# Optimization experiments

Measured on AMD Instinct MI355X. Metric: run time of the kernel, lower is better.

Reference implementation:

```python
import jax, jax.numpy as jnp
import numpy as np

N_NODES = 100000
N_EDGES = 1600000
IN_DIM = 3
LATENT = 128
LATENT_DEC = 128
NUM_LAYER = 2      # shared-weight middle GCN layers
NUM_LAYER_DEC = 2  # shared-weight middle decoder layers


def _glorot(key, shape):
    fan_in, fan_out = shape[0], shape[1]
    lim = np.sqrt(6.0 / (fan_in + fan_out)).astype(np.float32)
    return jax.random.uniform(key, shape, jnp.float32, -lim, lim)


def setup_inputs() -> dict:
    key = jax.random.key(0)
    ks = jax.random.split(key, 10)
    x = jax.random.normal(ks[0], (N_NODES, IN_DIM), jnp.float32)
    edge_index = jax.random.randint(ks[1], (2, N_EDGES), 0, N_NODES, jnp.int64)
    return {
        "x": x,
        "edge_index": edge_index,
        "W_s": _glorot(ks[2], (IN_DIM, LATENT)),   "b_s": jnp.zeros((LATENT,), jnp.float32),
        "W_m": _glorot(ks[3], (LATENT, LATENT)),   "b_m": jnp.zeros((LATENT,), jnp.float32),
        "W_e": _glorot(ks[4], (LATENT, LATENT)),   "b_e": jnp.zeros((LATENT,), jnp.float32),
        "W_sd": _glorot(ks[5], (LATENT, LATENT_DEC)),    "b_sd": jnp.zeros((LATENT_DEC,), jnp.float32),
        "W_md": _glorot(ks[6], (LATENT_DEC, LATENT_DEC)),"b_md": jnp.zeros((LATENT_DEC,), jnp.float32),
        "W_ed": _glorot(ks[7], (LATENT_DEC, IN_DIM)),    "b_ed": jnp.zeros((IN_DIM,), jnp.float32),
    }


def _gcn_conv(h, W, b, src, dst, dinv):
    # PyG GCNConv: out_i = sum_j norm_ij * (x_j @ W) + b, norm = d^-1/2_i d^-1/2_j
    h = h @ W
    norm = dinv[src] * dinv[dst]                       # [E+N]
    msg = norm[:, None] * h[src]                       # gather + scale
    out = jax.ops.segment_sum(msg, dst, num_segments=N_NODES)  # scatter-add
    return out + b


def reference(x, edge_index, W_s, b_s, W_m, b_m, W_e, b_e, W_sd, b_sd, W_md, b_md, W_ed, b_ed):
    loops = jnp.arange(N_NODES, dtype=edge_index.dtype)
    src = jnp.concatenate([edge_index[0], loops])      # add self-loops
    dst = jnp.concatenate([edge_index[1], loops])
    deg = jax.ops.segment_sum(jnp.ones(src.shape[0], x.dtype), dst, num_segments=N_NODES)
    dinv = jnp.where(deg > 0, jax.lax.rsqrt(deg), 0.0)

    h = jax.nn.relu(_gcn_conv(x, W_s, b_s, src, dst, dinv))
    for _ in range(NUM_LAYER):  # shared weights (ModuleList([layer]*n))
        h = jax.nn.relu(_gcn_conv(h, W_m, b_m, src, dst, dinv))
    h = jax.nn.relu(_gcn_conv(h, W_e, b_e, src, dst, dinv))

    h = jax.nn.relu(h @ W_sd + b_sd)
    for _ in range(NUM_LAYER_DEC):  # shared weights
        h = jax.nn.relu(h @ W_md + b_md)
    y = h @ W_ed + b_ed
    return y + x
```

## Files before the change

### kernel.cpp

```cpp
#include <hip/hip_runtime.h>


typedef __attribute__((ext_vector_type(8))) short short8;
typedef __attribute__((ext_vector_type(4))) float floatx4;
typedef __attribute__((ext_vector_type(2))) float floatx2;

#define BIN_CH 8192
#define NBMAX 512

__device__ __forceinline__ unsigned short f2bf(float f) {
    unsigned int u = __float_as_uint(f);
    u += 0x7fffu + ((u >> 16) & 1u);
    return (unsigned short)(u >> 16);
}
__device__ __forceinline__ float bflo(unsigned int u) { return __uint_as_float(u << 16); }
__device__ __forceinline__ float bfhi(unsigned int u) { return __uint_as_float(u & 0xffff0000u); }
__device__ __forceinline__ unsigned char f2fp8(float f) {
    return (unsigned char)(__builtin_amdgcn_cvt_pk_fp8_f32(f, f, 0, false) & 0xFF);
}


__global__ __launch_bounds__(512) void bin_kernel(
        const int* __restrict__ src, const int* __restrict__ dst,
        int* __restrict__ gfill, unsigned int* __restrict__ binbuf,
        int NB, int C, int E) {
    __shared__ int hist[NBMAX];
    __shared__ int start[NBMAX];
    __shared__ int dstoff[NBMAX];
    int tid = threadIdx.x;
    int e0 = blockIdx.x * BIN_CH;
    for (int i = tid; i < NB; i += 512) hist[i] = 0;
    __syncthreads();
    for (int i = tid; i < BIN_CH; i += 512) {
        int e = e0 + i;
        if (e < E) atomicAdd(&hist[dst[e] >> 9], 1);
    }
    __syncthreads();
    if (tid < 64) {
        int carry = 0;
        for (int base = 0; base < NB; base += 64) {
            int idx = base + tid;
            int v = (idx < NB) ? hist[idx] : 0;
            int s = v;
            #pragma unroll
            for (int off = 1; off < 64; off <<= 1) {
                int u = __shfl_up(s, off);
                if (tid >= off) s += u;
            }
            if (idx < NB) start[idx] = carry + s - v;
            carry += __shfl(s, 63);
        }
    }
    __syncthreads();
    for (int i = tid; i < NB; i += 512) {
        int cnt = hist[i];
        int g = cnt ? atomicAdd(&gfill[i], cnt) : 0;
        dstoff[i] = g - start[i];
        hist[i] = start[i];
    }
    __syncthreads();
    for (int i = tid; i < BIN_CH; i += 512) {
        int e = e0 + i;
        if (e >= E) continue;
        int d = dst[e];
        int b = d >> 9;
        int slot = atomicAdd(&hist[b], 1);
        int gidx = b * C + dstoff[b] + slot;
        if (gidx < (b + 1) * C)
            binbuf[gidx] = (unsigned int)src[e] | ((unsigned int)(d & 511) << 17);
    }
}

__global__ void bscan_kernel(const int* __restrict__ gfill, int* __restrict__ bbase, int NB) {
    int lane = threadIdx.x;
    int carry = 0;
    for (int base = 0; base < NB; base += 64) {
        int idx = base + lane;
        int v = (idx < NB) ? gfill[idx] : 0;
        int s = v;
        #pragma unroll
        for (int off = 1; off < 64; off <<= 1) {
            int u = __shfl_up(s, off);
            if (lane >= off) s += u;
        }
        if (idx < NB) bbase[idx] = carry + s - v;
        carry += __shfl(s, 63);
    }
}

__global__ __launch_bounds__(256) void build_kernel(
        const unsigned int* __restrict__ binbuf, const int* __restrict__ gfill,
        const int* __restrict__ bbase, int* __restrict__ rowptr,
        float* __restrict__ dinv, int* __restrict__ col,
        int NB, int C, int N, int E) {
    __shared__ int h[512];
    __shared__ int hs[512];
    int b = blockIdx.x, tid = threadIdx.x;
    int cnt = gfill[b];
    const unsigned int* p = binbuf + (size_t)b * C;
    for (int i = tid; i < 512; i += 256) h[i] = 0;
    __syncthreads();
    for (int i = tid; i < cnt; i += 256) atomicAdd(&h[p[i] >> 17], 1);
    __syncthreads();
    if (tid < 64) {
        int carry = 0;
        for (int base = 0; base < 512; base += 64) {
            int v = h[base + tid];
            int s = v;
            #pragma unroll
            for (int off = 1; off < 64; off <<= 1) {
                int u = __shfl_up(s, off);
                if (tid >= off) s += u;
            }
            hs[base + tid] = carry + s - v;
            carry += __shfl(s, 63);
        }
    }
    __syncthreads();
    int base = bbase[b];
    for (int i = tid; i < 512; i += 256) {
        int node = b * 512 + i;
        if (node < N) {
            rowptr[node] = base + hs[i];
            dinv[node] = 1.0f / sqrtf((float)(h[i] + 1));
        }
    }
    if (b == 0 && tid == 0) rowptr[N] = E;
    __syncthreads();
    for (int i = tid; i < cnt; i += 256) {
        unsigned int u = p[i];
        int local = u >> 17;
        int pos = atomicAdd(&hs[local], 1);
        col[base + pos] = (int)(u & 0x1FFFFu);
    }
}


__global__ void pack_kernel(const float* __restrict__ W0, const float* __restrict__ W1,
                            const float* __restrict__ W2, const float* __restrict__ W3,
                            unsigned short* __restrict__ P0, unsigned short* __restrict__ P1,
                            unsigned short* __restrict__ P2, unsigned short* __restrict__ P3) {
    int which = blockIdx.x >> 3;
    const float* W = which == 0 ? W0 : which == 1 ? W1 : which == 2 ? W2 : W3;
    unsigned short* P = which == 0 ? P0 : which == 1 ? P1 : which == 2 ? P2 : P3;
    int f = (blockIdx.x & 7) * 256 + threadIdx.x;
    int lane = f & 63, nt = (f >> 6) & 7, kc = f >> 9;
    int kbase = kc * 32 + (lane >> 4) * 8;
    int ncol = nt * 16 + (lane & 15);
    short8 frag;
    #pragma unroll
    for (int j = 0; j < 8; ++j)
        frag[j] = (short)f2bf(W[(size_t)(kbase + j) * 128 + ncol]);
    *((short8*)(P + (size_t)f * 8)) = frag;
}


__global__ void in_gemm_kernel(const float* __restrict__ x, const float* __restrict__ W,
                               const float* __restrict__ dinv,
                               unsigned char* __restrict__ t8, int n) {
    int g = blockIdx.x * 256 + threadIdx.x;
    int i = g >> 6, c2 = g & 63;
    if (i >= n) return;
    float x0 = x[i * 3], x1 = x[i * 3 + 1], x2 = x[i * 3 + 2];
    float d = dinv[i];
    int c = c2 * 2;
    float v0 = d * (x0 * W[c]     + x1 * W[128 + c]     + x2 * W[256 + c]);
    float v1 = d * (x0 * W[c + 1] + x1 * W[128 + c + 1] + x2 * W[256 + c + 1]);
    unsigned int pk = __builtin_amdgcn_cvt_pk_fp8_f32(v0, v1, 0, false);
    ((unsigned short*)t8)[(size_t)i * 64 + c2] = (unsigned short)(pk & 0xFFFF);
}


__global__ __launch_bounds__(256) void agg_kernel(
        const unsigned char* __restrict__ t8, const int* __restrict__ rowptr,
        const int* __restrict__ col, const float* __restrict__ dinv,
        const float* __restrict__ bias, unsigned short* __restrict__ out, int n) {
    int node = blockIdx.x * 16 + (threadIdx.x >> 4);
    int lane = threadIdx.x & 63;
    int q16 = lane >> 4;
    int lq  = lane & 15;
    if (node >= n) node = n - 1;
    floatx2 acc[4];
    #pragma unroll
    for (int i = 0; i < 4; ++i) acc[i] = (floatx2){0.f, 0.f};

    int beg = rowptr[node];
    int deg = rowptr[node + 1] - beg;
    for (int base = 0; base < deg; base += 16) {
        int m = deg - base;
        int jv = (lq < m) ? col[beg + base + lq] : n;
        #pragma unroll
        for (int eh = 0; eh < 2; ++eh) {
            uint2 v[8];
            #pragma unroll
            for (int q = 0; q < 8; ++q) {
                int j = __shfl(jv, q16 * 16 + eh * 8 + q);
                v[q] = ((const uint2*)(t8 + (size_t)j * 128))[lq];
            }
            #pragma unroll
            for (int q = 0; q < 8; ++q) {
                acc[0] += __builtin_amdgcn_cvt_pk_f32_fp8(v[q].x, false);
                acc[1] += __builtin_amdgcn_cvt_pk_f32_fp8(v[q].x, true);
                acc[2] += __builtin_amdgcn_cvt_pk_f32_fp8(v[q].y, false);
                acc[3] += __builtin_amdgcn_cvt_pk_f32_fp8(v[q].y, true);
            }
        }
    }
    uint2 s = ((const uint2*)(t8 + (size_t)node * 128))[lq];
    acc[0] += __builtin_amdgcn_cvt_pk_f32_fp8(s.x, false);
    acc[1] += __builtin_amdgcn_cvt_pk_f32_fp8(s.x, true);
    acc[2] += __builtin_amdgcn_cvt_pk_f32_fp8(s.y, false);
    acc[3] += __builtin_amdgcn_cvt_pk_f32_fp8(s.y, true);

    float di = dinv[node];
    const float4* b4 = (const float4*)bias;
    float4 b0 = b4[lq * 2], b1 = b4[lq * 2 + 1];
    float o0 = fmaxf(di * acc[0].x + b0.x, 0.f), o1 = fmaxf(di * acc[0].y + b0.y, 0.f);
    float o2 = fmaxf(di * acc[1].x + b0.z, 0.f), o3 = fmaxf(di * acc[1].y + b0.w, 0.f);
    float o4 = fmaxf(di * acc[2].x + b1.x, 0.f), o5 = fmaxf(di * acc[2].y + b1.y, 0.f);
    float o6 = fmaxf(di * acc[3].x + b1.z, 0.f), o7 = fmaxf(di * acc[3].y + b1.w, 0.f);
    uint4 o;
    o.x = (unsigned int)f2bf(o0) | ((unsigned int)f2bf(o1) << 16);
    o.y = (unsigned int)f2bf(o2) | ((unsigned int)f2bf(o3) << 16);
    o.z = (unsigned int)f2bf(o4) | ((unsigned int)f2bf(o5) << 16);
    o.w = (unsigned int)f2bf(o6) | ((unsigned int)f2bf(o7) << 16);
    ((uint4*)(out + (size_t)node * 128))[lq] = o;
}


template <bool ENC>
__global__ __launch_bounds__(256) void gemm_mfma_kernel(
        const unsigned short* __restrict__ A, const unsigned short* __restrict__ Wp,
        const float* __restrict__ bias, const float* __restrict__ dinv,
        void* __restrict__ outp, int n) {
    __shared__ unsigned short Ws[16384];
    int tid = threadIdx.x;
    {
        const int4* s = (const int4*)Wp;
        int4* d = (int4*)Ws;
        #pragma unroll
        for (int i = 0; i < 8; ++i) d[tid + 256 * i] = s[tid + 256 * i];
    }
    int wave = tid >> 6, lane = tid & 63;
    int quad = lane >> 4, mrow = lane & 15;
    int row0 = blockIdx.x * 128 + wave * 32;
    __syncthreads();

    short8 af[2][4];
    #pragma unroll
    for (int t = 0; t < 2; ++t) {
        int arow = row0 + t * 16 + mrow; if (arow >= n) arow = n - 1;
        const unsigned short* abase = A + (size_t)arow * 128 + quad * 8;
        #pragma unroll
        for (int kc = 0; kc < 4; ++kc)
            af[t][kc] = *((const short8*)(abase + kc * 32));
    }

    floatx4 acc[2][8];
    #pragma unroll
    for (int t = 0; t < 2; ++t)
        #pragma unroll
        for (int nt = 0; nt < 8; ++nt) acc[t][nt] = (floatx4){0.f, 0.f, 0.f, 0.f};

    #pragma unroll
    for (int kc = 0; kc < 4; ++kc) {
        #pragma unroll
        for (int nt = 0; nt < 8; ++nt) {
            short8 bf = *((const short8*)(Ws + ((kc * 8 + nt) * 64 + lane) * 8));
            acc[0][nt] = __builtin_amdgcn_mfma_f32_16x16x32_bf16(af[0][kc], bf, acc[0][nt], 0, 0, 0);
            acc[1][nt] = __builtin_amdgcn_mfma_f32_16x16x32_bf16(af[1][kc], bf, acc[1][nt], 0, 0, 0);
        }
    }

    #pragma unroll
    for (int t = 0; t < 2; ++t) {
        int rbase = row0 + t * 16 + quad * 4;
        float dv[4];
        if (ENC) {
            #pragma unroll
            for (int r = 0; r < 4; ++r)
                dv[r] = (rbase + r < n) ? dinv[rbase + r] : 0.f;
        }
        #pragma unroll
        for (int nt = 0; nt < 8; ++nt) {
            int colc = nt * 16 + mrow;
            float bcol = ENC ? 0.f : bias[colc];
            #pragma unroll
            for (int r = 0; r < 4; ++r) {
                int row = rbase + r;
                if (row < n) {
                    float v = acc[t][nt][r];
                    if (ENC) {
                        v *= dv[r];
                        ((unsigned char*)outp)[(size_t)row * 128 + colc] = f2fp8(v);
                    } else {
                        v = fmaxf(v + bcol, 0.f);
                        ((unsigned short*)outp)[(size_t)row * 128 + colc] = f2bf(v);
                    }
                }
            }
        }
    }
}


__global__ __launch_bounds__(256) void out_kernel(
        const unsigned short* __restrict__ h, const float* __restrict__ W,
        const float* __restrict__ bias, const float* __restrict__ x,
        float* __restrict__ out, int n) {
    int node = blockIdx.x * 4 + (threadIdx.x >> 6);
    int lane = threadIdx.x & 63;
    if (node >= n) return;
    unsigned int hv = ((const unsigned int*)(h + (size_t)node * 128))[lane];
    float h0 = bflo(hv), h1 = bfhi(hv);
    int c = lane * 2;
    float s0 = h0 * W[c * 3]     + h1 * W[(c + 1) * 3];
    float s1 = h0 * W[c * 3 + 1] + h1 * W[(c + 1) * 3 + 1];
    float s2 = h0 * W[c * 3 + 2] + h1 * W[(c + 1) * 3 + 2];
    #pragma unroll
    for (int off = 32; off > 0; off >>= 1) {
        s0 += __shfl_down(s0, off);
        s1 += __shfl_down(s1, off);
        s2 += __shfl_down(s2, off);
    }
    if (lane == 0) {
        out[node * 3 + 0] = s0 + bias[0] + x[node * 3 + 0];
        out[node * 3 + 1] = s1 + bias[1] + x[node * 3 + 1];
        out[node * 3 + 2] = s2 + bias[2] + x[node * 3 + 2];
    }
}


extern "C" void kernel_launch(void* const* d_in, const int* in_sizes, int n_in,
                              void* d_out, int out_size, void* d_ws, size_t ws_size,
                              hipStream_t stream) {
    const float* x    = (const float*)d_in[0];
    const int*   ei   = (const int*)d_in[1];
    const float* W_s  = (const float*)d_in[2];
    const float* b_s  = (const float*)d_in[3];
    const float* W_m  = (const float*)d_in[4];
    const float* b_m  = (const float*)d_in[5];
    const float* W_e  = (const float*)d_in[6];
    const float* b_e  = (const float*)d_in[7];
    const float* W_sd = (const float*)d_in[8];
    const float* b_sd = (const float*)d_in[9];
    const float* W_md = (const float*)d_in[10];
    const float* b_md = (const float*)d_in[11];
    const float* W_ed = (const float*)d_in[12];
    const float* b_ed = (const float*)d_in[13];
    float* outp = (float*)d_out;

    const int N = in_sizes[0] / 3;
    const int E = in_sizes[1] / 2;
    const int* src = ei;
    const int* dst = ei + E;

    const int NB = (N + 511) >> 9;
    const int C  = (((E / NB) * 3 / 2) + 255) & ~255;

    char* p = (char*)d_ws;
    auto carve = [&](size_t bytes) {
        void* r = (void*)p;
        p += (bytes + 255) & ~(size_t)255;
        return r;
    };
    int*   rowptr = (int*)  carve((size_t)(N + 1) * 4);
    int*   col    = (int*)  carve((size_t)E * 4);
    float* dinv   = (float*)carve((size_t)N * 4);
    int*   gfill  = (int*)  carve((size_t)NB * 4);
    int*   bbase  = (int*)  carve((size_t)NB * 4);
    unsigned int* binbuf = (unsigned int*)carve((size_t)NB * C * 4);
    unsigned short* Wp_m  = (unsigned short*)carve(16384 * 2);
    unsigned short* Wp_e  = (unsigned short*)carve(16384 * 2);
    unsigned short* Wp_sd = (unsigned short*)carve(16384 * 2);
    unsigned short* Wp_md = (unsigned short*)carve(16384 * 2);
    unsigned char*  T8 = (unsigned char*) carve((size_t)(N + 1) * 128);
    unsigned short* A  = (unsigned short*)carve((size_t)N * 128 * 2);
    unsigned short* Bm = (unsigned short*)carve((size_t)N * 128 * 2);
    (void)ws_size;

    const int gBin = (E + BIN_CH - 1) / BIN_CH;
    const int gNode4 = (N + 3) / 4;
    const int gNode16 = (N + 15) / 16;
    const int gRow128 = (N + 127) / 128;

    hipMemsetAsync(gfill, 0, (size_t)NB * 4, stream);
    hipMemsetAsync(T8 + (size_t)N * 128, 0, 128, stream);
    bin_kernel<<<gBin, 512, 0, stream>>>(src, dst, gfill, binbuf, NB, C, E);
    bscan_kernel<<<1, 64, 0, stream>>>(gfill, bbase, NB);
    build_kernel<<<NB, 256, 0, stream>>>(binbuf, gfill, bbase, rowptr, dinv, col, NB, C, N, E);

    pack_kernel<<<32, 256, 0, stream>>>(W_m, W_e, W_sd, W_md, Wp_m, Wp_e, Wp_sd, Wp_md);

    in_gemm_kernel<<<(N * 64 + 255) / 256, 256, 0, stream>>>(x, W_s, dinv, T8, N);
    agg_kernel<<<gNode16, 256, 0, stream>>>(T8, rowptr, col, dinv, b_s, A, N);

    gemm_mfma_kernel<true><<<gRow128, 256, 0, stream>>>(A, Wp_m, nullptr, dinv, T8, N);
    agg_kernel<<<gNode16, 256, 0, stream>>>(T8, rowptr, col, dinv, b_m, A, N);

    gemm_mfma_kernel<true><<<gRow128, 256, 0, stream>>>(A, Wp_m, nullptr, dinv, T8, N);
    agg_kernel<<<gNode16, 256, 0, stream>>>(T8, rowptr, col, dinv, b_m, A, N);

    gemm_mfma_kernel<true><<<gRow128, 256, 0, stream>>>(A, Wp_e, nullptr, dinv, T8, N);
    agg_kernel<<<gNode16, 256, 0, stream>>>(T8, rowptr, col, dinv, b_e, A, N);

    gemm_mfma_kernel<false><<<gRow128, 256, 0, stream>>>(A, Wp_sd, b_sd, nullptr, Bm, N);
    gemm_mfma_kernel<false><<<gRow128, 256, 0, stream>>>(Bm, Wp_md, b_md, nullptr, A, N);
    gemm_mfma_kernel<false><<<gRow128, 256, 0, stream>>>(A, Wp_md, b_md, nullptr, Bm, N);
    out_kernel<<<gNode4, 256, 0, stream>>>(Bm, W_ed, b_ed, x, outp, N);
}
```

Baseline: 440.7 us.

## Fuse aggregation with following GEMM and whole decoder into shared-memory tiles

Each GCN aggregation now writes its bf16 output tile to LDS, and the next layer's MFMA GEMM runs in the same block, emitting fp8 directly. This removes the intermediate bf16 global round trip. The decoder chain (final aggregation, three MLP layers and the output projection) becomes one kernel, and ping-pong T8 buffers replace the in-place buffer. The cost is fewer, larger blocks (128 nodes each) with much more LDS per block, which lowers occupancy during the latency-bound gather phase. The serialized 8-pass aggregation also loses parallelism.

```diff
diff --git a/kernel.cpp b/kernel.cpp
--- a/kernel.cpp
+++ b/kernel.cpp
@@ -7,16 +7,26 @@
 
 #define BIN_CH 8192
 #define NBMAX 512
+#define HS_STRIDE 68
 
 __device__ __forceinline__ unsigned short f2bf(float f) {
     unsigned int u = __float_as_uint(f);
     u += 0x7fffu + ((u >> 16) & 1u);
     return (unsigned short)(u >> 16);
 }
+__device__ __forceinline__ unsigned int pk_bf(float a, float b) {
+    return (unsigned int)f2bf(a) | ((unsigned int)f2bf(b) << 16);
+}
 __device__ __forceinline__ float bflo(unsigned int u) { return __uint_as_float(u << 16); }
 __device__ __forceinline__ float bfhi(unsigned int u) { return __uint_as_float(u & 0xffff0000u); }
 __device__ __forceinline__ unsigned char f2fp8(float f) {
     return (unsigned char)(__builtin_amdgcn_cvt_pk_fp8_f32(f, f, 0, false) & 0xFF);
+}
+__device__ __forceinline__ short8 ld_frag(const unsigned short* p) {
+    uint2 a = *(const uint2*)p;
+    uint2 b = *(const uint2*)(p + 4);
+    int4 v = make_int4((int)a.x, (int)a.y, (int)b.x, (int)b.y);
+    return __builtin_bit_cast(short8, v);
 }
 
 
@@ -171,97 +181,88 @@
 }
 
 
-__global__ __launch_bounds__(256) void agg_kernel(
+__device__ __forceinline__ void stage_ws(unsigned short* Ws, const unsigned short* Wp, int tid) {
+    const int4* s = (const int4*)Wp;
+    int4* d = (int4*)Ws;
+    #pragma unroll
+    for (int i = 0; i < 8; ++i) d[tid + 256 * i] = s[tid + 256 * i];
+}
+
+__device__ __forceinline__ void agg_phase(
         const unsigned char* __restrict__ t8, const int* __restrict__ rowptr,
         const int* __restrict__ col, const float* __restrict__ dinv,
-        const float* __restrict__ bias, unsigned short* __restrict__ out, int n) {
-    int node = blockIdx.x * 16 + (threadIdx.x >> 4);
-    int lane = threadIdx.x & 63;
+        const float* __restrict__ bias, unsigned short* Hs, int n, int tid) {
+    int lane = tid & 63;
+    int lq = lane & 15;
+    int sub = tid >> 4;
     int q16 = lane >> 4;
-    int lq  = lane & 15;
-    if (node >= n) node = n - 1;
-    floatx2 acc[4];
-    #pragma unroll
-    for (int i = 0; i < 4; ++i) acc[i] = (floatx2){0.f, 0.f};
-
-    int beg = rowptr[node];
-    int deg = rowptr[node + 1] - beg;
-    for (int base = 0; base < deg; base += 16) {
-        int m = deg - base;
-        int jv = (lq < m) ? col[beg + base + lq] : n;
-        #pragma unroll
-        for (int eh = 0; eh < 2; ++eh) {
-            uint2 v[8];
-            #pragma unroll
-            for (int q = 0; q < 8; ++q) {
-                int j = __shfl(jv, q16 * 16 + eh * 8 + q);
-                v[q] = ((const uint2*)(t8 + (size_t)j * 128))[lq];
-            }
-            #pragma unroll
-            for (int q = 0; q < 8; ++q) {
-                acc[0] += __builtin_amdgcn_cvt_pk_f32_fp8(v[q].x, false);
-                acc[1] += __builtin_amdgcn_cvt_pk_f32_fp8(v[q].x, true);
-                acc[2] += __builtin_amdgcn_cvt_pk_f32_fp8(v[q].y, false);
-                acc[3] += __builtin_amdgcn_cvt_pk_f32_fp8(v[q].y, true);
-            }
-        }
-    }
-    uint2 s = ((const uint2*)(t8 + (size_t)node * 128))[lq];
-    acc[0] += __builtin_amdgcn_cvt_pk_f32_fp8(s.x, false);
-    acc[1] += __builtin_amdgcn_cvt_pk_f32_fp8(s.x, true);
-    acc[2] += __builtin_amdgcn_cvt_pk_f32_fp8(s.y, false);
-    acc[3] += __builtin_amdgcn_cvt_pk_f32_fp8(s.y, true);
-
-    float di = dinv[node];
-    const float4* b4 = (const float4*)bias;
-    float4 b0 = b4[lq * 2], b1 = b4[lq * 2 + 1];
-    float o0 = fmaxf(di * acc[0].x + b0.x, 0.f), o1 = fmaxf(di * acc[0].y + b0.y, 0.f);
-    float o2 = fmaxf(di * acc[1].x + b0.z, 0.f), o3 = fmaxf(di * acc[1].y + b0.w, 0.f);
-    float o4 = fmaxf(di * acc[2].x + b1.x, 0.f), o5 = fmaxf(di * acc[2].y + b1.y, 0.f);
-    float o6 = fmaxf(di * acc[3].x + b1.z, 0.f), o7 = fmaxf(di * acc[3].y + b1.w, 0.f);
-    uint4 o;
-    o.x = (unsigned int)f2bf(o0) | ((unsigned int)f2bf(o1) << 16);
-    o.y = (unsigned int)f2bf(o2) | ((unsigned int)f2bf(o3) << 16);
-    o.z = (unsigned int)f2bf(o4) | ((unsigned int)f2bf(o5) << 16);
-    o.w = (unsigned int)f2bf(o6) | ((unsigned int)f2bf(o7) << 16);
-    ((uint4*)(out + (size_t)node * 128))[lq] = o;
-}
-
-
-template <bool ENC>
-__global__ __launch_bounds__(256) void gemm_mfma_kernel(
-        const unsigned short* __restrict__ A, const unsigned short* __restrict__ Wp,
-        const float* __restrict__ bias, const float* __restrict__ dinv,
-        void* __restrict__ outp, int n) {
-    __shared__ unsigned short Ws[16384];
-    int tid = threadIdx.x;
-    {
-        const int4* s = (const int4*)Wp;
-        int4* d = (int4*)Ws;
-        #pragma unroll
-        for (int i = 0; i < 8; ++i) d[tid + 256 * i] = s[tid + 256 * i];
-    }
-    int wave = tid >> 6, lane = tid & 63;
+    int nodebase = blockIdx.x * 128;
+    #pragma unroll 1
+    for (int pass = 0; pass < 8; ++pass) {
+        int nloc = pass * 16 + sub;
+        int node = nodebase + nloc;
+        if (node >= n) node = n - 1;
+        floatx2 acc[4];
+        #pragma unroll
+        for (int i = 0; i < 4; ++i) acc[i] = (floatx2){0.f, 0.f};
+        int beg = rowptr[node];
+        int deg = rowptr[node + 1] - beg;
+        for (int base = 0; base < deg; base += 16) {
+            int m = deg - base;
+            int jv = (lq < m) ? col[beg + base + lq] : n;
+            #pragma unroll
+            for (int eh = 0; eh < 2; ++eh) {
+                uint2 v[8];
+                #pragma unroll
+                for (int q = 0; q < 8; ++q) {
+                    int j = __shfl(jv, q16 * 16 + eh * 8 + q);
+                    v[q] = ((const uint2*)(t8 + (size_t)j * 128))[lq];
+                }
+                #pragma unroll
+                for (int q = 0; q < 8; ++q) {
+                    acc[0] += __builtin_amdgcn_cvt_pk_f32_fp8(v[q].x, false);
+                    acc[1] += __builtin_amdgcn_cvt_pk_f32_fp8(v[q].x, true);
+                    acc[2] += __builtin_amdgcn_cvt_pk_f32_fp8(v[q].y, false);
+                    acc[3] += __builtin_amdgcn_cvt_pk_f32_fp8(v[q].y, true);
+                }
+            }
+        }
+        uint2 s = ((const uint2*)(t8 + (size_t)node * 128))[lq];
+        acc[0] += __builtin_amdgcn_cvt_pk_f32_fp8(s.x, false);
+        acc[1] += __builtin_amdgcn_cvt_pk_f32_fp8(s.x, true);
+        acc[2] += __builtin_amdgcn_cvt_pk_f32_fp8(s.y, false);
+        acc[3] += __builtin_amdgcn_cvt_pk_f32_fp8(s.y, true);
+
+        float di = dinv[node];
+        const float4* b4 = (const float4*)bias;
+        float4 b0 = b4[lq * 2], b1 = b4[lq * 2 + 1];
+        float o0 = fmaxf(di * acc[0].x + b0.x, 0.f), o1 = fmaxf(di * acc[0].y + b0.y, 0.f);
+        float o2 = fmaxf(di * acc[1].x + b0.z, 0.f), o3 = fmaxf(di * acc[1].y + b0.w, 0.f);
+        float o4 = fmaxf(di * acc[2].x + b1.x, 0.f), o5 = fmaxf(di * acc[2].y + b1.y, 0.f);
+        float o6 = fmaxf(di * acc[3].x + b1.z, 0.f), o7 = fmaxf(di * acc[3].y + b1.w, 0.f);
+        unsigned short* hp = Hs + nloc * HS_STRIDE + lq * 8;
+        uint2 w0, w1;
+        w0.x = pk_bf(o0, o1); w0.y = pk_bf(o2, o3);
+        w1.x = pk_bf(o4, o5); w1.y = pk_bf(o6, o7);
+        *(uint2*)hp = w0;
+        *(uint2*)(hp + 4) = w1;
+    }
+}
+
+__device__ __forceinline__ void gemm_tile(
+        const unsigned short* Hs, const unsigned short* Ws,
+        int wav, int lane, floatx4 acc[2][8]) {
     int quad = lane >> 4, mrow = lane & 15;
-    int row0 = blockIdx.x * 128 + wave * 32;
-    __syncthreads();
-
     short8 af[2][4];
     #pragma unroll
-    for (int t = 0; t < 2; ++t) {
-        int arow = row0 + t * 16 + mrow; if (arow >= n) arow = n - 1;
-        const unsigned short* abase = A + (size_t)arow * 128 + quad * 8;
+    for (int t = 0; t < 2; ++t)
         #pragma unroll
         for (int kc = 0; kc < 4; ++kc)
-            af[t][kc] = *((const short8*)(abase + kc * 32));
-    }
-
-    floatx4 acc[2][8];
+            af[t][kc] = ld_frag(Hs + (wav * 32 + t * 16 + mrow) * HS_STRIDE + (kc * 4 + quad) * 8);
     #pragma unroll
     for (int t = 0; t < 2; ++t)
         #pragma unroll
         for (int nt = 0; nt < 8; ++nt) acc[t][nt] = (floatx4){0.f, 0.f, 0.f, 0.f};
-
     #pragma unroll
     for (int kc = 0; kc < 4; ++kc) {
         #pragma unroll
@@ -271,62 +272,135 @@
             acc[1][nt] = __builtin_amdgcn_mfma_f32_16x16x32_bf16(af[1][kc], bf, acc[1][nt], 0, 0, 0);
         }
     }
-
+}
+
+__device__ __forceinline__ void relu_store_hs(
+        unsigned short* Hs, const float* __restrict__ bias,
+        floatx4 acc[2][8], int wav, int lane) {
+    int quad = lane >> 4, mrow = lane & 15;
     #pragma unroll
     for (int t = 0; t < 2; ++t) {
-        int rbase = row0 + t * 16 + quad * 4;
-        float dv[4];
-        if (ENC) {
-            #pragma unroll
-            for (int r = 0; r < 4; ++r)
-                dv[r] = (rbase + r < n) ? dinv[rbase + r] : 0.f;
-        }
         #pragma unroll
         for (int nt = 0; nt < 8; ++nt) {
             int colc = nt * 16 + mrow;
-            float bcol = ENC ? 0.f : bias[colc];
+            float bcol = bias[colc];
+            #pragma unroll
+            for (int r = 0; r < 4; ++r) {
+                int rowl = wav * 32 + t * 16 + quad * 4 + r;
+                Hs[rowl * HS_STRIDE + colc] = f2bf(fmaxf(acc[t][nt][r] + bcol, 0.f));
+            }
+        }
+    }
+}
+
+
+__global__ __launch_bounds__(256) void agg_gemm_kernel(
+        const unsigned char* __restrict__ t8_in, const int* __restrict__ rowptr,
+        const int* __restrict__ col, const float* __restrict__ dinv,
+        const float* __restrict__ bias, const unsigned short* __restrict__ Wp,
+        unsigned char* __restrict__ t8_out, int n) {
+    __shared__ unsigned short Ws[16384];
+    __shared__ unsigned short Hs[128 * HS_STRIDE];
+    int tid = threadIdx.x;
+    stage_ws(Ws, Wp, tid);
+    agg_phase(t8_in, rowptr, col, dinv, bias, Hs, n, tid);
+    __syncthreads();
+
+    int wav = tid >> 6, lane = tid & 63;
+    int quad = lane >> 4, mrow = lane & 15;
+    floatx4 acc[2][8];
+    gemm_tile(Hs, Ws, wav, lane, acc);
+
+    int row0 = blockIdx.x * 128;
+    #pragma unroll
+    for (int t = 0; t < 2; ++t) {
+        int rbase = row0 + wav * 32 + t * 16 + quad * 4;
+        float dv[4];
+        #pragma unroll
+        for (int r = 0; r < 4; ++r)
+            dv[r] = (rbase + r < n) ? dinv[rbase + r] : 0.f;
+        #pragma unroll
+        for (int nt = 0; nt < 8; ++nt) {
+            int colc = nt * 16 + mrow;
             #pragma unroll
             for (int r = 0; r < 4; ++r) {
                 int row = rbase + r;
+                if (row < n)
+                    t8_out[(size_t)row * 128 + colc] = f2fp8(acc[t][nt][r] * dv[r]);
+            }
+        }
+    }
+}
+
+
+__global__ __launch_bounds__(256) void decoder_kernel(
+        const unsigned char* __restrict__ t8_in, const int* __restrict__ rowptr,
+        const int* __restrict__ col, const float* __restrict__ dinv,
+        const float* __restrict__ b_agg,
+        const unsigned short* __restrict__ Wp_sd, const float* __restrict__ b_sd,
+        const unsigned short* __restrict__ Wp_md, const float* __restrict__ b_md,
+        const float* __restrict__ W_ed, const float* __restrict__ b_ed,
+        const float* __restrict__ x, float* __restrict__ out, int n) {
+    __shared__ unsigned short Ws[16384];
+    __shared__ unsigned short Hs[128 * HS_STRIDE];
+    int tid = threadIdx.x;
+    stage_ws(Ws, Wp_sd, tid);
+    agg_phase(t8_in, rowptr, col, dinv, b_agg, Hs, n, tid);
+    __syncthreads();
+
+    int wav = tid >> 6, lane = tid & 63;
+    int quad = lane >> 4, mrow = lane & 15;
+    floatx4 acc[2][8];
+
+    gemm_tile(Hs, Ws, wav, lane, acc);
+    relu_store_hs(Hs, b_sd, acc, wav, lane);
+    __syncthreads();
+    stage_ws(Ws, Wp_md, tid);
+    __syncthreads();
+    gemm_tile(Hs, Ws, wav, lane, acc);
+    relu_store_hs(Hs, b_md, acc, wav, lane);
+    gemm_tile(Hs, Ws, wav, lane, acc);
+    #pragma unroll
+    for (int t = 0; t < 2; ++t)
+        #pragma unroll
+        for (int nt = 0; nt < 8; ++nt)
+            #pragma unroll
+            for (int r = 0; r < 4; ++r)
+                acc[t][nt][r] = fmaxf(acc[t][nt][r] + b_md[nt * 16 + mrow], 0.f);
+
+    float wed[8][3];
+    #pragma unroll
+    for (int nt = 0; nt < 8; ++nt) {
+        int c = nt * 16 + mrow;
+        #pragma unroll
+        for (int k = 0; k < 3; ++k) wed[nt][k] = W_ed[c * 3 + k];
+    }
+    int row0 = blockIdx.x * 128;
+    #pragma unroll
+    for (int t = 0; t < 2; ++t) {
+        #pragma unroll
+        for (int r = 0; r < 4; ++r) {
+            float s0 = 0.f, s1 = 0.f, s2 = 0.f;
+            #pragma unroll
+            for (int nt = 0; nt < 8; ++nt) {
+                float v = acc[t][nt][r];
+                s0 += v * wed[nt][0]; s1 += v * wed[nt][1]; s2 += v * wed[nt][2];
+            }
+            #pragma unroll
+            for (int off = 1; off < 16; off <<= 1) {
+                s0 += __shfl_xor(s0, off);
+                s1 += __shfl_xor(s1, off);
+                s2 += __shfl_xor(s2, off);
+            }
+            if (mrow == 0) {
+                int row = row0 + wav * 32 + t * 16 + quad * 4 + r;
                 if (row < n) {
-                    float v = acc[t][nt][r];
-                    if (ENC) {
-                        v *= dv[r];
-                        ((unsigned char*)outp)[(size_t)row * 128 + colc] = f2fp8(v);
-                    } else {
-                        v = fmaxf(v + bcol, 0.f);
-                        ((unsigned short*)outp)[(size_t)row * 128 + colc] = f2bf(v);
-                    }
+                    out[row * 3 + 0] = s0 + b_ed[0] + x[row * 3 + 0];
+                    out[row * 3 + 1] = s1 + b_ed[1] + x[row * 3 + 1];
+                    out[row * 3 + 2] = s2 + b_ed[2] + x[row * 3 + 2];
                 }
             }
         }
-    }
-}
-
-
-__global__ __launch_bounds__(256) void out_kernel(
-        const unsigned short* __restrict__ h, const float* __restrict__ W,
-        const float* __restrict__ bias, const float* __restrict__ x,
-        float* __restrict__ out, int n) {
-    int node = blockIdx.x * 4 + (threadIdx.x >> 6);
-    int lane = threadIdx.x & 63;
-    if (node >= n) return;
-    unsigned int hv = ((const unsigned int*)(h + (size_t)node * 128))[lane];
-    float h0 = bflo(hv), h1 = bfhi(hv);
-    int c = lane * 2;
-    float s0 = h0 * W[c * 3]     + h1 * W[(c + 1) * 3];
-    float s1 = h0 * W[c * 3 + 1] + h1 * W[(c + 1) * 3 + 1];
-    float s2 = h0 * W[c * 3 + 2] + h1 * W[(c + 1) * 3 + 2];
-    #pragma unroll
-    for (int off = 32; off > 0; off >>= 1) {
-        s0 += __shfl_down(s0, off);
-        s1 += __shfl_down(s1, off);
-        s2 += __shfl_down(s2, off);
-    }
-    if (lane == 0) {
-        out[node * 3 + 0] = s0 + bias[0] + x[node * 3 + 0];
-        out[node * 3 + 1] = s1 + bias[1] + x[node * 3 + 1];
-        out[node * 3 + 2] = s2 + bias[2] + x[node * 3 + 2];
     }
 }
 
@@ -374,38 +448,28 @@
     unsigned short* Wp_e  = (unsigned short*)carve(16384 * 2);
     unsigned short* Wp_sd = (unsigned short*)carve(16384 * 2);
     unsigned short* Wp_md = (unsigned short*)carve(16384 * 2);
-    unsigned char*  T8 = (unsigned char*) carve((size_t)(N + 1) * 128);
-    unsigned short* A  = (unsigned short*)carve((size_t)N * 128 * 2);
-    unsigned short* Bm = (unsigned short*)carve((size_t)N * 128 * 2);
+    unsigned char*  T8a = (unsigned char*)carve((size_t)(N + 1) * 128);
+    unsigned char*  T8b = (unsigned char*)carve((size_t)(N + 1) * 128);
     (void)ws_size;
 
     const int gBin = (E + BIN_CH - 1) / BIN_CH;
-    const int gNode4 = (N + 3) / 4;
-    const int gNode16 = (N + 15) / 16;
-    const int gRow128 = (N + 127) / 128;
+    const int gTile = (N + 127) / 128;
 
     hipMemsetAsync(gfill, 0, (size_t)NB * 4, stream);
-    hipMemsetAsync(T8 + (size_t)N * 128, 0, 128, stream);
+    hipMemsetAsync(T8a + (size_t)N * 128, 0, 128, stream);
+    hipMemsetAsync(T8b + (size_t)N * 128, 0, 128, stream);
     bin_kernel<<<gBin, 512, 0, stream>>>(src, dst, gfill, binbuf, NB, C, E);
     bscan_kernel<<<1, 64, 0, stream>>>(gfill, bbase, NB);
     build_kernel<<<NB, 256, 0, stream>>>(binbuf, gfill, bbase, rowptr, dinv, col, NB, C, N, E);
 
     pack_kernel<<<32, 256, 0, stream>>>(W_m, W_e, W_sd, W_md, Wp_m, Wp_e, Wp_sd, Wp_md);
 
-    in_gemm_kernel<<<(N * 64 + 255) / 256, 256, 0, stream>>>(x, W_s, dinv, T8, N);
-    agg_kernel<<<gNode16, 256, 0, stream>>>(T8, rowptr, col, dinv, b_s, A, N);
-
-    gemm_mfma_kernel<true><<<gRow128, 256, 0, stream>>>(A, Wp_m, nullptr, dinv, T8, N);
-    agg_kernel<<<gNode16, 256, 0, stream>>>(T8, rowptr, col, dinv, b_m, A, N);
-
-    gemm_mfma_kernel<true><<<gRow128, 256, 0, stream>>>(A, Wp_m, nullptr, dinv, T8, N);
-    agg_kernel<<<gNode16, 256, 0, stream>>>(T8, rowptr, col, dinv, b_m, A, N);
-
-    gemm_mfma_kernel<true><<<gRow128, 256, 0, stream>>>(A, Wp_e, nullptr, dinv, T8, N);
-    agg_kernel<<<gNode16, 256, 0, stream>>>(T8, rowptr, col, dinv, b_e, A, N);
-
-    gemm_mfma_kernel<false><<<gRow128, 256, 0, stream>>>(A, Wp_sd, b_sd, nullptr, Bm, N);
-    gemm_mfma_kernel<false><<<gRow128, 256, 0, stream>>>(Bm, Wp_md, b_md, nullptr, A, N);
-    gemm_mfma_kernel<false><<<gRow128, 256, 0, stream>>>(A, Wp_md, b_md, nullptr, Bm, N);
-    out_kernel<<<gNode4, 256, 0, stream>>>(Bm, W_ed, b_ed, x, outp, N);
-}
+    in_gemm_kernel<<<(N * 64 + 255) / 256, 256, 0, stream>>>(x, W_s, dinv, T8a, N);
+    agg_gemm_kernel<<<gTile, 256, 0, stream>>>(T8a, rowptr, col, dinv, b_s, Wp_m, T8b, N);
+    agg_gemm_kernel<<<gTile, 256, 0, stream>>>(T8b, rowptr, col, dinv, b_m, Wp_m, T8a, N);
+    agg_gemm_kernel<<<gTile, 256, 0, stream>>>(T8a, rowptr, col, dinv, b_m, Wp_e, T8b, N);
+
+    decoder_kernel<<<gTile, 256, 0, stream>>>(T8b, rowptr, col, dinv, b_e,
+                                              Wp_sd, b_sd, Wp_md, b_md,
+                                              W_ed, b_ed, x, outp, N);
+}
```

Result: slower. 457.1 us (+3.7%).

## Sort nodes into degree classes to balance work in aggregation kernel

Applied to the files above, without the earlier changes.

Adds count and place kernels that bucket nodes by degree (in 16-edge chunks) into a permutation array. The aggregation kernel then processes nodes in permuted order, so nodes grouped in a wavefront have similar degrees and loop trip counts. The aim is to cut divergence and load imbalance in the gather loop. The cost is two extra small kernels, an indirection, and less locality for output writes and rowptr reads.

```diff
diff --git a/kernel.cpp b/kernel.cpp
--- a/kernel.cpp
+++ b/kernel.cpp
@@ -132,6 +132,71 @@
         int local = u >> 17;
         int pos = atomicAdd(&hs[local], 1);
         col[base + pos] = (int)(u & 0x1FFFFu);
+    }
+}
+
+
+__global__ __launch_bounds__(256) void ccount_kernel(
+        const int* __restrict__ rowptr, int* __restrict__ ccount, int N) {
+    __shared__ int lc[32];
+    int tid = threadIdx.x;
+    if (tid < 32) lc[tid] = 0;
+    __syncthreads();
+    int i0 = blockIdx.x * 2048 + tid;
+    #pragma unroll
+    for (int k = 0; k < 8; ++k) {
+        int i = i0 + k * 256;
+        if (i < N) {
+            int deg = rowptr[i + 1] - rowptr[i];
+            int c = (deg + 15) >> 4; if (c > 31) c = 31;
+            atomicAdd(&lc[c], 1);
+        }
+    }
+    __syncthreads();
+    if (tid < 32 && lc[tid]) atomicAdd(&ccount[tid], lc[tid]);
+}
+
+__global__ __launch_bounds__(256) void cplace_kernel(
+        const int* __restrict__ rowptr, const int* __restrict__ ccount,
+        int* __restrict__ ccur, int* __restrict__ perm, int N) {
+    __shared__ int cb[32];
+    __shared__ int lc[32];
+    __shared__ int lbase[32];
+    int tid = threadIdx.x;
+    if (tid < 32) {
+        lc[tid] = 0;
+        int s = 0;
+        for (int k = 0; k < 32; ++k) { if (k == tid) break; s += ccount[k]; }
+        cb[tid] = s;
+    }
+    __syncthreads();
+    int i0 = blockIdx.x * 2048 + tid;
+    int cls[8];
+    #pragma unroll
+    for (int k = 0; k < 8; ++k) {
+        int i = i0 + k * 256;
+        cls[k] = -1;
+        if (i < N) {
+            int deg = rowptr[i + 1] - rowptr[i];
+            int c = (deg + 15) >> 4; if (c > 31) c = 31;
+            cls[k] = c;
+            atomicAdd(&lc[c], 1);
+        }
+    }
+    __syncthreads();
+    if (tid < 32) {
+        int cnt = lc[tid];
+        lbase[tid] = cnt ? atomicAdd(&ccur[tid], cnt) : 0;
+        lc[tid] = 0;
+    }
+    __syncthreads();
+    #pragma unroll
+    for (int k = 0; k < 8; ++k) {
+        int i = i0 + k * 256;
+        if (cls[k] >= 0) {
+            int slot = atomicAdd(&lc[cls[k]], 1);
+            perm[cb[cls[k]] + lbase[cls[k]] + slot] = i;
+        }
     }
 }
 
@@ -174,12 +239,14 @@
 __global__ __launch_bounds__(256) void agg_kernel(
         const unsigned char* __restrict__ t8, const int* __restrict__ rowptr,
         const int* __restrict__ col, const float* __restrict__ dinv,
-        const float* __restrict__ bias, unsigned short* __restrict__ out, int n) {
-    int node = blockIdx.x * 16 + (threadIdx.x >> 4);
+        const float* __restrict__ bias, const int* __restrict__ perm,
+        unsigned short* __restrict__ out, int n) {
+    int gidx = blockIdx.x * 16 + (threadIdx.x >> 4);
+    if (gidx >= n) gidx = n - 1;
+    int node = perm[gidx];
     int lane = threadIdx.x & 63;
     int q16 = lane >> 4;
     int lq  = lane & 15;
-    if (node >= n) node = n - 1;
     floatx2 acc[4];
     #pragma unroll
     for (int i = 0; i < 4; ++i) acc[i] = (floatx2){0.f, 0.f};
@@ -369,6 +436,8 @@
     float* dinv   = (float*)carve((size_t)N * 4);
     int*   gfill  = (int*)  carve((size_t)NB * 4);
     int*   bbase  = (int*)  carve((size_t)NB * 4);
+    int*   cmeta  = (int*)  carve(64 * 4);
+    int*   perm   = (int*)  carve((size_t)N * 4);
     unsigned int* binbuf = (unsigned int*)carve((size_t)NB * C * 4);
     unsigned short* Wp_m  = (unsigned short*)carve(16384 * 2);
     unsigned short* Wp_e  = (unsigned short*)carve(16384 * 2);
@@ -379,30 +448,37 @@
     unsigned short* Bm = (unsigned short*)carve((size_t)N * 128 * 2);
     (void)ws_size;
 
+    int* ccount = cmeta;
+    int* ccur   = cmeta + 32;
+
     const int gBin = (E + BIN_CH - 1) / BIN_CH;
     const int gNode4 = (N + 3) / 4;
     const int gNode16 = (N + 15) / 16;
     const int gRow128 = (N + 127) / 128;
+    const int gCls = (N + 2047) / 2048;
 
     hipMemsetAsync(gfill, 0, (size_t)NB * 4, stream);
+    hipMemsetAsync(cmeta, 0, 64 * 4, stream);
     hipMemsetAsync(T8 + (size_t)N * 128, 0, 128, stream);
     bin_kernel<<<gBin, 512, 0, stream>>>(src, dst, gfill, binbuf, NB, C, E);
     bscan_kernel<<<1, 64, 0, stream>>>(gfill, bbase, NB);
     build_kernel<<<NB, 256, 0, stream>>>(binbuf, gfill, bbase, rowptr, dinv, col, NB, C, N, E);
+    ccount_kernel<<<gCls, 256, 0, stream>>>(rowptr, ccount, N);
+    cplace_kernel<<<gCls, 256, 0, stream>>>(rowptr, ccount, ccur, perm, N);
 
     pack_kernel<<<32, 256, 0, stream>>>(W_m, W_e, W_sd, W_md, Wp_m, Wp_e, Wp_sd, Wp_md);
 
     in_gemm_kernel<<<(N * 64 + 255) / 256, 256, 0, stream>>>(x, W_s, dinv, T8, N);
-    agg_kernel<<<gNode16, 256, 0, stream>>>(T8, rowptr, col, dinv, b_s, A, N);
+    agg_kernel<<<gNode16, 256, 0, stream>>>(T8, rowptr, col, dinv, b_s, perm, A, N);
 
     gemm_mfma_kernel<true><<<gRow128, 256, 0, stream>>>(A, Wp_m, nullptr, dinv, T8, N);
-    agg_kernel<<<gNode16, 256, 0, stream>>>(T8, rowptr, col, dinv, b_m, A, N);
+    agg_kernel<<<gNode16, 256, 0, stream>>>(T8, rowptr, col, dinv, b_m, perm, A, N);
 
     gemm_mfma_kernel<true><<<gRow128, 256, 0, stream>>>(A, Wp_m, nullptr, dinv, T8, N);
-    agg_kernel<<<gNode16, 256, 0, stream>>>(T8, rowptr, col, dinv, b_m, A, N);
+    agg_kernel<<<gNode16, 256, 0, stream>>>(T8, rowptr, col, dinv, b_m, perm, A, N);
 
     gemm_mfma_kernel<true><<<gRow128, 256, 0, stream>>>(A, Wp_e, nullptr, dinv, T8, N);
-    agg_kernel<<<gNode16, 256, 0, stream>>>(T8, rowptr, col, dinv, b_e, A, N);
+    agg_kernel<<<gNode16, 256, 0, stream>>>(T8, rowptr, col, dinv, b_e, perm, A, N);
 
     gemm_mfma_kernel<false><<<gRow128, 256, 0, stream>>>(A, Wp_sd, b_sd, nullptr, Bm, N);
     gemm_mfma_kernel<false><<<gRow128, 256, 0, stream>>>(Bm, Wp_md, b_md, nullptr, A, N);
```

After: 447.9 us. Within noise of the previous version (+1.6%).

## Widen aggregation gathers to 16B and fuse last decoder GEMM with output layer

Applied to the files above, without the earlier changes.

The aggregation kernel now has each lane load 16 bytes of an fp8 neighbor row, with two half-groups each handling alternate edges, and combines the partial sums with an xor shuffle before writing bf16. This halves the number of gather instructions per edge and widens each memory request. Separately, the final decoder MFMA GEMM is fused with the 128->3 projection, bias and residual add, which removes one bf16 intermediate write and read plus a kernel launch. The cost is more accumulator registers, an extra cross-lane reduction in agg, and a shuffle reduction in the fused epilogue.

```diff
diff --git a/kernel.cpp b/kernel.cpp
--- a/kernel.cpp
+++ b/kernel.cpp
@@ -12,6 +12,9 @@
     unsigned int u = __float_as_uint(f);
     u += 0x7fffu + ((u >> 16) & 1u);
     return (unsigned short)(u >> 16);
+}
+__device__ __forceinline__ unsigned int pk_bf(float a, float b) {
+    return (unsigned int)f2bf(a) | ((unsigned int)f2bf(b) << 16);
 }
 __device__ __forceinline__ float bflo(unsigned int u) { return __uint_as_float(u << 16); }
 __device__ __forceinline__ float bfhi(unsigned int u) { return __uint_as_float(u & 0xffff0000u); }
@@ -179,52 +182,71 @@
     int lane = threadIdx.x & 63;
     int q16 = lane >> 4;
     int lq  = lane & 15;
+    int oct = (lane >> 3) & 1;
+    int l8  = lane & 7;
     if (node >= n) node = n - 1;
-    floatx2 acc[4];
-    #pragma unroll
-    for (int i = 0; i < 4; ++i) acc[i] = (floatx2){0.f, 0.f};
+    floatx2 acc[8];
+    #pragma unroll
+    for (int i = 0; i < 8; ++i) acc[i] = (floatx2){0.f, 0.f};
 
     int beg = rowptr[node];
     int deg = rowptr[node + 1] - beg;
     for (int base = 0; base < deg; base += 16) {
         int m = deg - base;
         int jv = (lq < m) ? col[beg + base + lq] : n;
-        #pragma unroll
-        for (int eh = 0; eh < 2; ++eh) {
-            uint2 v[8];
-            #pragma unroll
-            for (int q = 0; q < 8; ++q) {
-                int j = __shfl(jv, q16 * 16 + eh * 8 + q);
-                v[q] = ((const uint2*)(t8 + (size_t)j * 128))[lq];
-            }
-            #pragma unroll
-            for (int q = 0; q < 8; ++q) {
-                acc[0] += __builtin_amdgcn_cvt_pk_f32_fp8(v[q].x, false);
-                acc[1] += __builtin_amdgcn_cvt_pk_f32_fp8(v[q].x, true);
-                acc[2] += __builtin_amdgcn_cvt_pk_f32_fp8(v[q].y, false);
-                acc[3] += __builtin_amdgcn_cvt_pk_f32_fp8(v[q].y, true);
-            }
-        }
-    }
-    uint2 s = ((const uint2*)(t8 + (size_t)node * 128))[lq];
+        uint4 v[8];
+        #pragma unroll
+        for (int q = 0; q < 8; ++q) {
+            int j = __shfl(jv, q16 * 16 + q * 2 + oct);
+            v[q] = ((const uint4*)(t8 + (size_t)j * 128))[l8];
+        }
+        #pragma unroll
+        for (int q = 0; q < 8; ++q) {
+            acc[0] += __builtin_amdgcn_cvt_pk_f32_fp8(v[q].x, false);
+            acc[1] += __builtin_amdgcn_cvt_pk_f32_fp8(v[q].x, true);
+            acc[2] += __builtin_amdgcn_cvt_pk_f32_fp8(v[q].y, false);
+            acc[3] += __builtin_amdgcn_cvt_pk_f32_fp8(v[q].y, true);
+            acc[4] += __builtin_amdgcn_cvt_pk_f32_fp8(v[q].z, false);
+            acc[5] += __builtin_amdgcn_cvt_pk_f32_fp8(v[q].z, true);
+            acc[6] += __builtin_amdgcn_cvt_pk_f32_fp8(v[q].w, false);
+            acc[7] += __builtin_amdgcn_cvt_pk_f32_fp8(v[q].w, true);
+        }
+    }
+    #pragma unroll
+    for (int i = 0; i < 8; ++i) {
+        acc[i].x += __shfl_xor(acc[i].x, 8);
+        acc[i].y += __shfl_xor(acc[i].y, 8);
+    }
+    uint4 s = ((const uint4*)(t8 + (size_t)node * 128))[l8];
     acc[0] += __builtin_amdgcn_cvt_pk_f32_fp8(s.x, false);
     acc[1] += __builtin_amdgcn_cvt_pk_f32_fp8(s.x, true);
     acc[2] += __builtin_amdgcn_cvt_pk_f32_fp8(s.y, false);
     acc[3] += __builtin_amdgcn_cvt_pk_f32_fp8(s.y, true);
+    acc[4] += __builtin_amdgcn_cvt_pk_f32_fp8(s.z, false);
+    acc[5] += __builtin_amdgcn_cvt_pk_f32_fp8(s.z, true);
+    acc[6] += __builtin_amdgcn_cvt_pk_f32_fp8(s.w, false);
+    acc[7] += __builtin_amdgcn_cvt_pk_f32_fp8(s.w, true);
 
     float di = dinv[node];
     const float4* b4 = (const float4*)bias;
-    float4 b0 = b4[lq * 2], b1 = b4[lq * 2 + 1];
-    float o0 = fmaxf(di * acc[0].x + b0.x, 0.f), o1 = fmaxf(di * acc[0].y + b0.y, 0.f);
-    float o2 = fmaxf(di * acc[1].x + b0.z, 0.f), o3 = fmaxf(di * acc[1].y + b0.w, 0.f);
-    float o4 = fmaxf(di * acc[2].x + b1.x, 0.f), o5 = fmaxf(di * acc[2].y + b1.y, 0.f);
-    float o6 = fmaxf(di * acc[3].x + b1.z, 0.f), o7 = fmaxf(di * acc[3].y + b1.w, 0.f);
-    uint4 o;
-    o.x = (unsigned int)f2bf(o0) | ((unsigned int)f2bf(o1) << 16);
-    o.y = (unsigned int)f2bf(o2) | ((unsigned int)f2bf(o3) << 16);
-    o.z = (unsigned int)f2bf(o4) | ((unsigned int)f2bf(o5) << 16);
-    o.w = (unsigned int)f2bf(o6) | ((unsigned int)f2bf(o7) << 16);
-    ((uint4*)(out + (size_t)node * 128))[lq] = o;
+    float o[16];
+    #pragma unroll
+    for (int k = 0; k < 4; ++k) {
+        float4 bb = b4[l8 * 4 + k];
+        o[k*4+0] = fmaxf(di * acc[k*2].x   + bb.x, 0.f);
+        o[k*4+1] = fmaxf(di * acc[k*2].y   + bb.y, 0.f);
+        o[k*4+2] = fmaxf(di * acc[k*2+1].x + bb.z, 0.f);
+        o[k*4+3] = fmaxf(di * acc[k*2+1].y + bb.w, 0.f);
+    }
+    if (oct == 0) {
+        uint4 w0, w1;
+        w0.x = pk_bf(o[0],  o[1]);  w0.y = pk_bf(o[2],  o[3]);
+        w0.z = pk_bf(o[4],  o[5]);  w0.w = pk_bf(o[6],  o[7]);
+        w1.x = pk_bf(o[8],  o[9]);  w1.y = pk_bf(o[10], o[11]);
+        w1.z = pk_bf(o[12], o[13]); w1.w = pk_bf(o[14], o[15]);
+        ((uint4*)(out + (size_t)node * 128))[l8 * 2]     = w0;
+        ((uint4*)(out + (size_t)node * 128))[l8 * 2 + 1] = w1;
+    }
 }
 
 
@@ -304,29 +326,82 @@
 }
 
 
-__global__ __launch_bounds__(256) void out_kernel(
-        const unsigned short* __restrict__ h, const float* __restrict__ W,
-        const float* __restrict__ bias, const float* __restrict__ x,
+__global__ __launch_bounds__(256) void gemm_out_kernel(
+        const unsigned short* __restrict__ A, const unsigned short* __restrict__ Wp,
+        const float* __restrict__ bias, const float* __restrict__ W_ed,
+        const float* __restrict__ b_ed, const float* __restrict__ x,
         float* __restrict__ out, int n) {
-    int node = blockIdx.x * 4 + (threadIdx.x >> 6);
-    int lane = threadIdx.x & 63;
-    if (node >= n) return;
-    unsigned int hv = ((const unsigned int*)(h + (size_t)node * 128))[lane];
-    float h0 = bflo(hv), h1 = bfhi(hv);
-    int c = lane * 2;
-    float s0 = h0 * W[c * 3]     + h1 * W[(c + 1) * 3];
-    float s1 = h0 * W[c * 3 + 1] + h1 * W[(c + 1) * 3 + 1];
-    float s2 = h0 * W[c * 3 + 2] + h1 * W[(c + 1) * 3 + 2];
-    #pragma unroll
-    for (int off = 32; off > 0; off >>= 1) {
-        s0 += __shfl_down(s0, off);
-        s1 += __shfl_down(s1, off);
-        s2 += __shfl_down(s2, off);
-    }
-    if (lane == 0) {
-        out[node * 3 + 0] = s0 + bias[0] + x[node * 3 + 0];
-        out[node * 3 + 1] = s1 + bias[1] + x[node * 3 + 1];
-        out[node * 3 + 2] = s2 + bias[2] + x[node * 3 + 2];
+    __shared__ unsigned short Ws[16384];
+    int tid = threadIdx.x;
+    {
+        const int4* s = (const int4*)Wp;
+        int4* d = (int4*)Ws;
+        #pragma unroll
+        for (int i = 0; i < 8; ++i) d[tid + 256 * i] = s[tid + 256 * i];
+    }
+    int wave = tid >> 6, lane = tid & 63;
+    int quad = lane >> 4, mrow = lane & 15;
+    int row0 = blockIdx.x * 128 + wave * 32;
+    __syncthreads();
+
+    short8 af[2][4];
+    #pragma unroll
+    for (int t = 0; t < 2; ++t) {
+        int arow = row0 + t * 16 + mrow; if (arow >= n) arow = n - 1;
+        const unsigned short* abase = A + (size_t)arow * 128 + quad * 8;
+        #pragma unroll
+        for (int kc = 0; kc < 4; ++kc)
+            af[t][kc] = *((const short8*)(abase + kc * 32));
+    }
+
+    floatx4 acc[2][8];
+    #pragma unroll
+    for (int t = 0; t < 2; ++t)
+        #pragma unroll
+        for (int nt = 0; nt < 8; ++nt) acc[t][nt] = (floatx4){0.f, 0.f, 0.f, 0.f};
+
+    #pragma unroll
+    for (int kc = 0; kc < 4; ++kc) {
+        #pragma unroll
+        for (int nt = 0; nt < 8; ++nt) {
+            short8 bf = *((const short8*)(Ws + ((kc * 8 + nt) * 64 + lane) * 8));
+            acc[0][nt] = __builtin_amdgcn_mfma_f32_16x16x32_bf16(af[0][kc], bf, acc[0][nt], 0, 0, 0);
+            acc[1][nt] = __builtin_amdgcn_mfma_f32_16x16x32_bf16(af[1][kc], bf, acc[1][nt], 0, 0, 0);
+        }
+    }
+
+    float wed[8][3];
+    #pragma unroll
+    for (int nt = 0; nt < 8; ++nt) {
+        int c = nt * 16 + mrow;
+        #pragma unroll
+        for (int k = 0; k < 3; ++k) wed[nt][k] = W_ed[c * 3 + k];
+    }
+    #pragma unroll
+    for (int t = 0; t < 2; ++t) {
+        #pragma unroll
+        for (int r = 0; r < 4; ++r) {
+            float s0 = 0.f, s1 = 0.f, s2 = 0.f;
+            #pragma unroll
+            for (int nt = 0; nt < 8; ++nt) {
+                float v = fmaxf(acc[t][nt][r] + bias[nt * 16 + mrow], 0.f);
+                s0 += v * wed[nt][0]; s1 += v * wed[nt][1]; s2 += v * wed[nt][2];
+            }
+            #pragma unroll
+            for (int off = 1; off < 16; off <<= 1) {
+                s0 += __shfl_xor(s0, off);
+                s1 += __shfl_xor(s1, off);
+                s2 += __shfl_xor(s2, off);
+            }
+            if (mrow == 0) {
+                int row = row0 + t * 16 + quad * 4 + r;
+                if (row < n) {
+                    out[row * 3 + 0] = s0 + b_ed[0] + x[row * 3 + 0];
+                    out[row * 3 + 1] = s1 + b_ed[1] + x[row * 3 + 1];
+                    out[row * 3 + 2] = s2 + b_ed[2] + x[row * 3 + 2];
+                }
+            }
+        }
     }
 }
 
@@ -380,7 +455,6 @@
     (void)ws_size;
 
     const int gBin = (E + BIN_CH - 1) / BIN_CH;
-    const int gNode4 = (N + 3) / 4;
     const int gNode16 = (N + 15) / 16;
     const int gRow128 = (N + 127) / 128;
 
@@ -406,6 +480,5 @@
 
     gemm_mfma_kernel<false><<<gRow128, 256, 0, stream>>>(A, Wp_sd, b_sd, nullptr, Bm, N);
     gemm_mfma_kernel<false><<<gRow128, 256, 0, stream>>>(Bm, Wp_md, b_md, nullptr, A, N);
-    gemm_mfma_kernel<false><<<gRow128, 256, 0, stream>>>(A, Wp_md, b_md, nullptr, Bm, N);
-    out_kernel<<<gNode4, 256, 0, stream>>>(Bm, W_ed, b_ed, x, outp, N);
-}
+    gemm_out_kernel<<<gRow128, 256, 0, stream>>>(A, Wp_md, b_md, W_ed, b_ed, x, outp, N);
+}
```

Result: faster. 430.3 us (-2.4%).
